# Performance work log

Measured on AMD Instinct MI355X. Metric: run time of the kernel, lower is better.

## Reference

```python
import jax, jax.numpy as jnp
import numpy as np

N, D, H, F = 50000, 128, 8, 512
HD = D // H
EPS_BN = 1e-5


def _batchnorm(x, gamma, beta):
    # BatchNorm1d in training mode: per-feature batch stats over node dim
    m = x.mean(axis=0)
    v = x.var(axis=0)
    return (x - m) * jax.lax.rsqrt(v + EPS_BN) * gamma + beta


def setup_inputs() -> dict:
    key = jax.random.key(0)
    ks = jax.random.split(key, 12)
    s = 0.05
    return {
        "src": jax.random.normal(ks[0], (N, D), jnp.float32),
        "edge_index": jax.random.randint(ks[1], (2, 800000), 0, N, jnp.int64),
        "q_w": jax.random.normal(ks[2], (D, D), jnp.float32) * s,
        "q_b": jnp.zeros((D,), jnp.float32),
        "k_w": jax.random.normal(ks[3], (D, D), jnp.float32) * s,
        "v_w": jax.random.normal(ks[4], (D, D), jnp.float32) * s,
        "out_w": jax.random.normal(ks[5], (D, D), jnp.float32) * s,
        "out_b": jnp.zeros((D,), jnp.float32),
        "g1": jnp.ones((D,), jnp.float32),
        "b1": jnp.zeros((D,), jnp.float32),
        "lin1_w": jax.random.normal(ks[6], (F, D), jnp.float32) * s,
        "lin1_b": jnp.zeros((F,), jnp.float32),
        "lin2_w": jax.random.normal(ks[7], (D, F), jnp.float32) * s,
        "lin2_b": jnp.zeros((D,), jnp.float32),
        "g2": jnp.ones((D,), jnp.float32),
        "b2": jnp.zeros((D,), jnp.float32),
    }


def reference(src, edge_index, q_w, q_b, k_w, v_w, out_w, out_b,
              g1, b1, lin1_w, lin1_b, lin2_w, lin2_b, g2, b2):
    n = src.shape[0]
    # add self loops, then attention edge index is (dst=edge[1], src=edge[0])
    loops = jnp.arange(n, dtype=edge_index.dtype)
    ei = jnp.concatenate([edge_index, jnp.stack([loops, loops])], axis=1)
    e_src, e_dst = ei[0], ei[1]  # message flows e_src -> e_dst; query index = e_dst

    scaling = float(HD) ** (-0.5)
    q = ((src @ q_w.T + q_b) * scaling).reshape(n, H, HD)
    k = (src @ k_w.T).reshape(n, H, HD)
    v = (src @ v_w.T).reshape(n, H, HD)

    # per-edge scores [E, H]
    w = jnp.einsum("ehd,ehd->eh", q[e_dst], k[e_src])
    # deterministic segment softmax over edges grouped by destination node
    mx = jax.ops.segment_max(w, e_dst, num_segments=n)
    ex = jnp.exp(w - mx[e_dst])
    den = jax.ops.segment_sum(ex, e_dst, num_segments=n)
    attn_w = ex / (den[e_dst] + 1e-16)  # [E, H]

    # weighted scatter-add aggregation -> [n, H, HD]
    msgs = attn_w[:, :, None] * v[e_src]
    agg = jax.ops.segment_sum(msgs, e_dst, num_segments=n)

    attn_out = agg.reshape(n, D) @ out_w.T + out_b
    x = _batchnorm(src + attn_out, g1, b1)

    ff = jax.nn.leaky_relu(x @ lin1_w.T + lin1_b, negative_slope=0.01)
    ff = ff @ lin2_w.T + lin2_b
    x = _batchnorm(x + ff, g2, b2)
    return x
```

## Files before the change

kernel.cpp:

```cpp
#include <hip/hip_runtime.h>
#include <math.h>

#define D 128
#define H 8
#define HD 16

typedef __attribute__((ext_vector_type(8))) short bf16x8;
typedef __attribute__((ext_vector_type(4))) float f32x4;

__device__ __forceinline__ ushort f2bf(float x) {
    union { float f; unsigned u; } v; v.f = x;
    unsigned r = v.u + 0x7fffu + ((v.u >> 16) & 1u);
    return (ushort)(r >> 16);
}
__device__ __forceinline__ float bflo(unsigned u) {
    union { unsigned u; float f; } x; x.u = u << 16; return x.f;
}
__device__ __forceinline__ float bfhi(unsigned u) {
    union { unsigned u; float f; } x; x.u = u & 0xffff0000u; return x.f;
}
__device__ __forceinline__ float bf2f(short s) {
    union { unsigned u; float f; } x; x.u = ((unsigned)(ushort)s) << 16; return x.f;
}

__device__ __forceinline__ float dot16(const float* qf, uint4 a, uint4 b) {
    float w;
    w  = qf[0]  * bflo(a.x) + qf[1]  * bfhi(a.x);
    w += qf[2]  * bflo(a.y) + qf[3]  * bfhi(a.y);
    w += qf[4]  * bflo(a.z) + qf[5]  * bfhi(a.z);
    w += qf[6]  * bflo(a.w) + qf[7]  * bfhi(a.w);
    w += qf[8]  * bflo(b.x) + qf[9]  * bfhi(b.x);
    w += qf[10] * bflo(b.y) + qf[11] * bfhi(b.y);
    w += qf[12] * bflo(b.z) + qf[13] * bfhi(b.z);
    w += qf[14] * bflo(b.w) + qf[15] * bfhi(b.w);
    return w;
}
__device__ __forceinline__ void acc16(float* num, float e, uint4 a, uint4 b) {
    num[0]  = fmaf(e, bflo(a.x), num[0]);  num[1]  = fmaf(e, bfhi(a.x), num[1]);
    num[2]  = fmaf(e, bflo(a.y), num[2]);  num[3]  = fmaf(e, bfhi(a.y), num[3]);
    num[4]  = fmaf(e, bflo(a.z), num[4]);  num[5]  = fmaf(e, bfhi(a.z), num[5]);
    num[6]  = fmaf(e, bflo(a.w), num[6]);  num[7]  = fmaf(e, bfhi(a.w), num[7]);
    num[8]  = fmaf(e, bflo(b.x), num[8]);  num[9]  = fmaf(e, bfhi(b.x), num[9]);
    num[10] = fmaf(e, bflo(b.y), num[10]); num[11] = fmaf(e, bfhi(b.y), num[11]);
    num[12] = fmaf(e, bflo(b.z), num[12]); num[13] = fmaf(e, bfhi(b.z), num[13]);
    num[14] = fmaf(e, bflo(b.w), num[14]); num[15] = fmaf(e, bfhi(b.w), num[15]);
}

template<int EPI, int M>
__global__ __launch_bounds__(256)
void gemm_v4_kernel(const ushort* __restrict__ A,
                    const ushort* __restrict__ W,
                    const float* __restrict__ bias,
                    const float* __restrict__ extf,
                    ushort* __restrict__ outb, int N)
{
    const int lane = threadIdx.x & 63, wave = threadIdx.x >> 6;
    const int lr = lane & 15, lq = lane >> 4;
    const int colbase = blockIdx.y * 128 + wave * 32;

    bf16x8 bfr[2][4];
    {
        const ushort* wp = W + (size_t)(colbase + lr) * 128 + lq * 8;
        #pragma unroll
        for (int ct = 0; ct < 2; ++ct)
            #pragma unroll
            for (int t = 0; t < 4; ++t)
                bfr[ct][t] = *(const bf16x8*)(wp + (size_t)ct * 16 * 128 + t * 32);
    }
    float biasv[2];
    biasv[0] = bias[colbase + lr];
    biasv[1] = bias[colbase + 16 + lr];

    const int stride = gridDim.x * 32;
    int r0 = blockIdx.x * 32;
    if (r0 >= N) return;

    bf16x8 cur[2][4], nxt[2][4];
    auto loadA = [&](int rb, bf16x8 (&dst)[2][4]) {
        #pragma unroll
        for (int s = 0; s < 2; ++s) {
            int ar = min(rb + s * 16 + lr, N - 1);
            const ushort* ap = A + (size_t)ar * 128 + lq * 8;
            #pragma unroll
            for (int t = 0; t < 4; ++t)
                dst[s][t] = *(const bf16x8*)(ap + t * 32);
        }
    };
    loadA(r0, cur);

    while (true) {
        int rn = r0 + stride;
        if (rn < N) loadA(rn, nxt);

        f32x4 acc[2][2] = {};
        #pragma unroll
        for (int t = 0; t < 4; ++t) {
            acc[0][0] = __builtin_amdgcn_mfma_f32_16x16x32_bf16(cur[0][t], bfr[0][t], acc[0][0], 0, 0, 0);
            acc[1][0] = __builtin_amdgcn_mfma_f32_16x16x32_bf16(cur[1][t], bfr[0][t], acc[1][0], 0, 0, 0);
            acc[0][1] = __builtin_amdgcn_mfma_f32_16x16x32_bf16(cur[0][t], bfr[1][t], acc[0][1], 0, 0, 0);
            acc[1][1] = __builtin_amdgcn_mfma_f32_16x16x32_bf16(cur[1][t], bfr[1][t], acc[1][1], 0, 0, 0);
        }

        #pragma unroll
        for (int ct = 0; ct < 2; ++ct) {
            int gcol = colbase + ct * 16 + lr;
            #pragma unroll
            for (int s = 0; s < 2; ++s) {
                #pragma unroll
                for (int r = 0; r < 4; ++r) {
                    int grow = r0 + s * 16 + lq * 4 + r;
                    if (grow >= N) continue;
                    size_t o = (size_t)grow * M + gcol;
                    float v = acc[s][ct][r] + biasv[ct];
                    if (EPI == 2)      v = v > 0.f ? v : 0.01f * v;
                    else if (EPI == 3) v += extf[o];
                    outb[o] = f2bf(v);
                }
            }
        }

        if (rn >= N) break;
        r0 = rn;
        #pragma unroll
        for (int s = 0; s < 2; ++s)
            #pragma unroll
            for (int t = 0; t < 4; ++t) cur[s][t] = nxt[s][t];
    }
}

template<int K, int MW>
__global__ __launch_bounds__(256)
void gemm_v2_kernel(const ushort* __restrict__ Ap,
                    const ushort* __restrict__ W,
                    const float* __restrict__ bias,
                    const ushort* __restrict__ extb,
                    const float* __restrict__ rawstats,
                    const float* __restrict__ gg,
                    const float* __restrict__ bb,
                    ushort* __restrict__ outb,
                    int N)
{
    constexpr int M   = MW * 4;
    constexpr int KC  = 128;
    constexpr int KT  = KC / 32;
    constexpr int NKC = K / KC;

    const int lane = threadIdx.x & 63, wave = threadIdx.x >> 6;
    const int lr = lane & 15, lq = lane >> 4;
    const int row0 = blockIdx.x * 32;
    const int c0w  = wave * MW;

    int ar0 = min(row0 + lr, N - 1);
    int ar1 = min(row0 + 16 + lr, N - 1);

    bf16x8 afr[2][KT];
    auto loadA = [&](int kc) {
        #pragma unroll
        for (int s = 0; s < 2; ++s) {
            int ar = s ? ar1 : ar0;
            const ushort* ap = Ap + (size_t)ar * K + kc * KC + lq * 8;
            #pragma unroll
            for (int t = 0; t < KT; ++t) afr[s][t] = *(const bf16x8*)(ap + t * 32);
        }
    };

    f32x4 acc[2][2] = {};
    #pragma unroll 1
    for (int kc = 0; kc < NKC; ++kc) {
        loadA(kc);
        const ushort* wp0 = W + (size_t)(c0w + lr) * K + kc * KC + lq * 8;
        const ushort* wp1 = wp0 + (size_t)16 * K;
        #pragma unroll
        for (int t = 0; t < KT; ++t) {
            bf16x8 b0 = *(const bf16x8*)(wp0 + t * 32);
            bf16x8 b1 = *(const bf16x8*)(wp1 + t * 32);
            acc[0][0] = __builtin_amdgcn_mfma_f32_16x16x32_bf16(afr[0][t], b0, acc[0][0], 0, 0, 0);
            acc[1][0] = __builtin_amdgcn_mfma_f32_16x16x32_bf16(afr[1][t], b0, acc[1][0], 0, 0, 0);
            acc[0][1] = __builtin_amdgcn_mfma_f32_16x16x32_bf16(afr[0][t], b1, acc[0][1], 0, 0, 0);
            acc[1][1] = __builtin_amdgcn_mfma_f32_16x16x32_bf16(afr[1][t], b1, acc[1][1], 0, 0, 0);
        }
    }

    #pragma unroll
    for (int ct = 0; ct < 2; ++ct) {
        int col = c0w + ct * 16 + lr;
        float biasv = bias[col];
        float mean = rawstats[col] / (float)N;
        float var  = rawstats[128 + col] / (float)N - mean * mean;
        float scv = gg[col] * rsqrtf(var + 1e-5f);
        float shv = bb[col] - mean * scv;
        #pragma unroll
        for (int s = 0; s < 2; ++s) {
            #pragma unroll
            for (int r = 0; r < 4; ++r) {
                int grow = row0 + s * 16 + lq * 4 + r;
                if (grow >= N) continue;
                size_t o = (size_t)grow * M + col;
                float v = acc[s][ct][r] + biasv + fmaf(bf2f((short)extb[o]), scv, shv);
                outb[o] = f2bf(v);
            }
        }
    }
}

__global__ __launch_bounds__(256)
void convert_deg_kernel(const float* __restrict__ qw, const float* __restrict__ qb,
                        const float* __restrict__ kw, const float* __restrict__ vw,
                        const float* __restrict__ ow, const float* __restrict__ w1,
                        const float* __restrict__ w2,
                        ushort* __restrict__ wqkv, ushort* __restrict__ wout,
                        ushort* __restrict__ w1b, ushort* __restrict__ w2b,
                        float* __restrict__ bqkv,
                        const float* __restrict__ src, ushort* __restrict__ srcbf,
                        int nd8,
                        const int* __restrict__ ei, long long E0,
                        int* __restrict__ deg)
{
    long long i = (long long)blockIdx.x * 256 + threadIdx.x;
    if (i < E0) atomicAdd(&deg[ei[E0 + i]], 1);
    if (i < nd8) {
        const float4* sp = (const float4*)(src + i * 8);
        float4 f0 = sp[0], f1 = sp[1];
        ushort u[8];
        u[0]=f2bf(f0.x); u[1]=f2bf(f0.y); u[2]=f2bf(f0.z); u[3]=f2bf(f0.w);
        u[4]=f2bf(f1.x); u[5]=f2bf(f1.y); u[6]=f2bf(f1.z); u[7]=f2bf(f1.w);
        *(uint4*)(srcbf + i * 8) = *(uint4*)u;
    }
    if (i < 49152) {
        int row = (int)i >> 7;
        float v;
        if (row < 128)      v = 0.25f * qw[i];
        else if (row < 256) v = kw[i - 16384];
        else                v = vw[i - 32768];
        wqkv[i] = f2bf(v);
        return;
    }
    long long j = i - 49152;
    if (j < 16384) { wout[j] = f2bf(ow[j]); return; }
    j -= 16384;
    if (j < 65536) { w1b[j] = f2bf(w1[j]); return; }
    j -= 65536;
    if (j < 65536) { w2b[j] = f2bf(w2[j]); return; }
    j -= 65536;
    if (j < 384) bqkv[j] = (j < 128) ? 0.25f * qb[j] : 0.f;
}

__global__ __launch_bounds__(256)
void w1fold_kernel(const ushort* __restrict__ w1b, const float* __restrict__ lb1,
                   const float* __restrict__ rawstats,
                   const float* __restrict__ g1, const float* __restrict__ b1,
                   ushort* __restrict__ w1f, float* __restrict__ bias1f, int N)
{
    int f = blockIdx.x * 4 + (threadIdx.x >> 6);
    int lane = threadIdx.x & 63;
    int k0 = lane * 2;
    float m0 = rawstats[k0] / (float)N;
    float v0 = rawstats[128 + k0] / (float)N - m0 * m0;
    float sc0 = g1[k0] * rsqrtf(v0 + 1e-5f);
    float sh0 = b1[k0] - m0 * sc0;
    float m1 = rawstats[k0 + 1] / (float)N;
    float v1 = rawstats[128 + k0 + 1] / (float)N - m1 * m1;
    float sc1 = g1[k0 + 1] * rsqrtf(v1 + 1e-5f);
    float sh1 = b1[k0 + 1] - m1 * sc1;

    uint wp = *(const uint*)(w1b + (size_t)f * 128 + k0);
    float w0 = bflo(wp), w1v = bfhi(wp);
    uint o = (uint)f2bf(w0 * sc0) | ((uint)f2bf(w1v * sc1) << 16);
    *(uint*)(w1f + (size_t)f * 128 + k0) = o;

    float part = w0 * sh0 + w1v * sh1;
    #pragma unroll
    for (int m = 1; m < 64; m <<= 1) part += __shfl_xor(part, m, 64);
    if (lane == 0) bias1f[f] = lb1[f] + part;
}

__global__ __launch_bounds__(256)
void scan_block_sum(const int* __restrict__ deg, int n, int* __restrict__ bsum)
{
    __shared__ int sh[256];
    int i = blockIdx.x * 256 + threadIdx.x;
    sh[threadIdx.x] = (i < n) ? deg[i] : 0;
    __syncthreads();
    for (int ofs = 128; ofs > 0; ofs >>= 1) {
        if (threadIdx.x < ofs) sh[threadIdx.x] += sh[threadIdx.x + ofs];
        __syncthreads();
    }
    if (threadIdx.x == 0) bsum[blockIdx.x] = sh[0];
}

__global__ __launch_bounds__(256)
void scan_final(const int* __restrict__ deg, int n, const int* __restrict__ bsum,
                int nb, int* __restrict__ rowptr)
{
    __shared__ int sb[256];
    __shared__ int sh[256];
    int t = threadIdx.x;
    sb[t] = (t < nb) ? bsum[t] : 0;
    __syncthreads();
    for (int ofs = 1; ofs < 256; ofs <<= 1) {
        int v = (t >= ofs) ? sb[t - ofs] : 0;
        __syncthreads();
        sb[t] += v;
        __syncthreads();
    }
    int boff = (blockIdx.x == 0) ? 0 : sb[blockIdx.x - 1];

    int i = blockIdx.x * 256 + t;
    int v = (i < n) ? deg[i] : 0;
    sh[t] = v;
    __syncthreads();
    for (int ofs = 1; ofs < 256; ofs <<= 1) {
        int u = (t >= ofs) ? sh[t - ofs] : 0;
        __syncthreads();
        sh[t] += u;
        __syncthreads();
    }
    if (i < n) rowptr[i] = boff + sh[t] - v;
    if (i == n - 1) rowptr[n] = boff + sh[t];
}

__global__ __launch_bounds__(256)
void scatter_kernel(const int* __restrict__ ei, long long E0,
                    const int* __restrict__ rowptr, int* __restrict__ cnt,
                    int* __restrict__ col)
{
    long long e = (long long)blockIdx.x * 256 + threadIdx.x;
    if (e >= E0) return;
    int s = ei[e], d = ei[E0 + e];
    int pos = rowptr[d] + atomicAdd(&cnt[d], 1);
    col[pos] = s;
}

__global__ __launch_bounds__(256)
void gat_agg_kernel(const int* __restrict__ rowptr, const int* __restrict__ col,
                    const ushort* __restrict__ qkv, ushort* __restrict__ agg, int N)
{
    int node = blockIdx.x * 4 + (threadIdx.x >> 6);
    if (node >= N) return;
    int lane = threadIdx.x & 63;
    int es = lane >> 3, h = lane & 7;
    const uint4* Q = (const uint4*)qkv;

    const uint4* qp = Q + (size_t)node * 48 + h * 2;
    uint4 qa = qp[0], qb = qp[1];
    float qf[16];
    qf[0]=bflo(qa.x); qf[1]=bfhi(qa.x); qf[2]=bflo(qa.y); qf[3]=bfhi(qa.y);
    qf[4]=bflo(qa.z); qf[5]=bfhi(qa.z); qf[6]=bflo(qa.w); qf[7]=bfhi(qa.w);
    qf[8]=bflo(qb.x); qf[9]=bfhi(qb.x); qf[10]=bflo(qb.y); qf[11]=bfhi(qb.y);
    qf[12]=bflo(qb.z); qf[13]=bfhi(qb.z); qf[14]=bflo(qb.w); qf[15]=bfhi(qb.w);

    float num[16];
    #pragma unroll
    for (int i = 0; i < 16; i++) num[i] = 0.f;
    float den = 0.f;

    int beg = rowptr[node];
    int total = rowptr[node + 1] - beg + 1;
    for (int idx = es; idx < total; idx += 8) {
        int s = (idx == 0) ? node : col[beg + idx - 1];
        const uint4* rp = Q + (size_t)s * 48 + h * 2;
        uint4 ka = rp[16], kb = rp[17], va = rp[32], vb = rp[33];
        float ev = __expf(dot16(qf, ka, kb));
        den += ev;
        acc16(num, ev, va, vb);
    }

    #pragma unroll
    for (int m = 8; m < 64; m <<= 1) {
        den += __shfl_xor(den, m, 64);
        #pragma unroll
        for (int i = 0; i < 16; i++) num[i] += __shfl_xor(num[i], m, 64);
    }

    if (es == 0) {
        float inv = 1.f / (den + 1e-16f);
        uint4 o0, o1;
        o0.x = (uint)f2bf(num[0]*inv)  | ((uint)f2bf(num[1]*inv)  << 16);
        o0.y = (uint)f2bf(num[2]*inv)  | ((uint)f2bf(num[3]*inv)  << 16);
        o0.z = (uint)f2bf(num[4]*inv)  | ((uint)f2bf(num[5]*inv)  << 16);
        o0.w = (uint)f2bf(num[6]*inv)  | ((uint)f2bf(num[7]*inv)  << 16);
        o1.x = (uint)f2bf(num[8]*inv)  | ((uint)f2bf(num[9]*inv)  << 16);
        o1.y = (uint)f2bf(num[10]*inv) | ((uint)f2bf(num[11]*inv) << 16);
        o1.z = (uint)f2bf(num[12]*inv) | ((uint)f2bf(num[13]*inv) << 16);
        o1.w = (uint)f2bf(num[14]*inv) | ((uint)f2bf(num[15]*inv) << 16);
        uint4* op = (uint4*)(agg + (size_t)node * 128 + h * 16);
        op[0] = o0; op[1] = o1;
    }
}

__global__ __launch_bounds__(256)
void bn_stats_bf16_kernel(const ushort* __restrict__ y, int N, float* __restrict__ stats)
{
    int jp = threadIdx.x & 63;
    int q4 = threadIdx.x >> 6;
    int r = blockIdx.x * 256 + q4;
    int rend = min(N, (int)(blockIdx.x + 1) * 256);
    float s0 = 0.f, qq0 = 0.f, s1 = 0.f, qq1 = 0.f;
    const uint* yp = (const uint*)y;
    for (; r < rend; r += 4) {
        uint u = yp[(size_t)r * 64 + jp];
        float a = bflo(u), b = bfhi(u);
        s0 += a; qq0 += a * a; s1 += b; qq1 += b * b;
    }
    __shared__ float sh[4][64][4];
    sh[q4][jp][0] = s0; sh[q4][jp][1] = qq0; sh[q4][jp][2] = s1; sh[q4][jp][3] = qq1;
    __syncthreads();
    if (threadIdx.x < 128) {
        int p = threadIdx.x >> 1;
        int w = threadIdx.x & 1;
        float ss = 0.f, sq = 0.f;
        #pragma unroll
        for (int i = 0; i < 4; i++) { ss += sh[i][p][w * 2]; sq += sh[i][p][w * 2 + 1]; }
        unsafeAtomicAdd(&stats[2 * p + w], ss);
        unsafeAtomicAdd(&stats[128 + 2 * p + w], sq);
    }
}

__global__ __launch_bounds__(256)
void bn_apply_out_kernel(const ushort* __restrict__ y, const float* __restrict__ rawstats,
                         const float* __restrict__ g, const float* __restrict__ b,
                         float* __restrict__ out, int total4, int N)
{
    __shared__ float scs[128], shs[128];
    if (threadIdx.x < 128) {
        int j = threadIdx.x;
        float mean = rawstats[j] / (float)N;
        float var  = rawstats[128 + j] / (float)N - mean * mean;
        float sc = g[j] * rsqrtf(var + 1e-5f);
        scs[j] = sc;
        shs[j] = b[j] - mean * sc;
    }
    __syncthreads();
    int i = blockIdx.x * 256 + threadIdx.x;
    if (i >= total4) return;
    uint2 u = reinterpret_cast<const uint2*>(y)[i];
    int j = (i * 4) & (D - 1);
    float4 v;
    v.x = bflo(u.x) * scs[j + 0] + shs[j + 0];
    v.y = bfhi(u.x) * scs[j + 1] + shs[j + 1];
    v.z = bflo(u.y) * scs[j + 2] + shs[j + 2];
    v.w = bfhi(u.y) * scs[j + 3] + shs[j + 3];
    reinterpret_cast<float4*>(out)[i] = v;
}

extern "C" void kernel_launch(void* const* d_in, const int* in_sizes, int n_in,
                              void* d_out, int out_size, void* d_ws, size_t ws_size,
                              hipStream_t stream)
{
    const float* src    = (const float*)d_in[0];
    const int*   ei     = (const int*)  d_in[1];
    const float* q_w    = (const float*)d_in[2];
    const float* q_b    = (const float*)d_in[3];
    const float* k_w    = (const float*)d_in[4];
    const float* v_w    = (const float*)d_in[5];
    const float* out_w  = (const float*)d_in[6];
    const float* out_b  = (const float*)d_in[7];
    const float* g1     = (const float*)d_in[8];
    const float* b1     = (const float*)d_in[9];
    const float* lin1_w = (const float*)d_in[10];
    const float* lin1_b = (const float*)d_in[11];
    const float* lin2_w = (const float*)d_in[12];
    const float* lin2_b = (const float*)d_in[13];
    const float* g2     = (const float*)d_in[14];
    const float* b2     = (const float*)d_in[15];

    const int N        = in_sizes[0] / D;
    const long long E0 = in_sizes[1] / 2;

    float* ws = (float*)d_ws;
    size_t off = 0;
    ushort* qkv   = (ushort*)(ws + off); off += (size_t)N * 192;
    ushort* agg   = (ushort*)(ws + off); off += (size_t)N * 64;
    ushort* srcbf = (ushort*)(ws + off); off += (size_t)N * 64;
    ushort* y1b   = (ushort*)(ws + off); off += (size_t)N * 64;
    ushort* hid   = (ushort*)(ws + off); off += (size_t)N * 256;
    ushort* y2b   = (ushort*)(ws + off); off += (size_t)N * 64;
    ushort* wqkv  = (ushort*)(ws + off); off += 24576;
    ushort* woutb = (ushort*)(ws + off); off += 8192;
    ushort* w1b   = (ushort*)(ws + off); off += 32768;
    ushort* w1f   = (ushort*)(ws + off); off += 32768;
    ushort* w2b   = (ushort*)(ws + off); off += 32768;
    float*  bqkv  = ws + off;            off += 384;
    float*  bias1f= ws + off;            off += 512;
    size_t zero_start = off;
    int* deg    = (int*)(ws + off); off += N;
    int* cnt    = (int*)(ws + off); off += N;
    float* stats1 = ws + off; off += 512;
    float* stats2 = ws + off; off += 512;
    size_t zero_cnt = off - zero_start;
    int* rowptr = (int*)(ws + off); off += N + 1;
    int* bsum   = (int*)(ws + off); off += 256;
    int* col    = (int*)(ws + off); off += E0;

    hipMemsetAsync(ws + zero_start, 0, zero_cnt * sizeof(float), stream);

    dim3 blk(256);

    dim3 gE0((unsigned)((E0 + 255) / 256));
    hipLaunchKernelGGL(convert_deg_kernel, gE0, blk, 0, stream,
                       q_w, q_b, k_w, v_w, out_w, lin1_w, lin2_w,
                       wqkv, woutb, w1b, w2b, bqkv,
                       src, srcbf, N * 16, ei, E0, deg);

    int nb = (N + 255) / 256;
    hipLaunchKernelGGL(scan_block_sum, dim3(nb), blk, 0, stream, deg, N, bsum);
    hipLaunchKernelGGL(scan_final, dim3(nb), blk, 0, stream, deg, N, bsum, nb, rowptr);
    hipLaunchKernelGGL(scatter_kernel, gE0, blk, 0, stream, ei, E0, rowptr, cnt, col);

    const int gx = 1024;

    hipLaunchKernelGGL((gemm_v4_kernel<0, 384>), dim3(gx, 3), blk, 0, stream,
                       srcbf, wqkv, bqkv, nullptr, qkv, N);

    hipLaunchKernelGGL(gat_agg_kernel, dim3((N + 3) / 4), blk, 0, stream,
                       rowptr, col, qkv, agg, N);

    hipLaunchKernelGGL((gemm_v4_kernel<3, 128>), dim3(gx, 1), blk, 0, stream,
                       agg, woutb, out_b, src, y1b, N);

    dim3 gS((N + 255) / 256);
    hipLaunchKernelGGL(bn_stats_bf16_kernel, gS, blk, 0, stream, y1b, N, stats1);

    hipLaunchKernelGGL(w1fold_kernel, dim3(128), blk, 0, stream,
                       w1b, lin1_b, stats1, g1, b1, w1f, bias1f, N);

    hipLaunchKernelGGL((gemm_v4_kernel<2, 512>), dim3(gx, 4), blk, 0, stream,
                       y1b, w1f, bias1f, nullptr, hid, N);

    hipLaunchKernelGGL((gemm_v2_kernel<512, 32>), dim3((N + 31) / 32), blk, 0, stream,
                       hid, w2b, lin2_b, y1b, stats1, g1, b1, y2b, N);

    hipLaunchKernelGGL(bn_stats_bf16_kernel, gS, blk, 0, stream, y2b, N, stats2);
    int total4 = N * D / 4;
    hipLaunchKernelGGL(bn_apply_out_kernel, dim3((total4 + 255) / 256), blk, 0, stream,
                       y2b, stats2, g2, b2, (float*)d_out, total4, N);
}
```

Measured before the change: 452.5 us.

## Fuse BatchNorm statistics into GEMM epilogues and rewrite lin2 as persistent kernel

Per-column sum and sum-of-squares are now accumulated in the epilogues of the out-projection GEMM and a new lin2 kernel, then reduced with wave shuffles and atomics. This removes both separate bn_stats passes over the bf16 activations. The lin2 GEMM becomes a persistent, grid-strided kernel that keeps all 512 K-values of W in registers and double-buffers A loads, where the old version reloaded weights for every row tile. The stats are taken from the fp32 values before bf16 rounding, so they can differ slightly from statistics computed on the stored bf16 data. Heavier register use may lower occupancy.

```diff
diff --git a/kernel.cpp b/kernel.cpp
--- a/kernel.cpp
+++ b/kernel.cpp
@@ -46,13 +46,15 @@
     num[14] = fmaf(e, bflo(b.w), num[14]); num[15] = fmaf(e, bfhi(b.w), num[15]);
 }
 
-template<int EPI, int M>
+template<int EPI, int M, int STATS>
 __global__ __launch_bounds__(256)
 void gemm_v4_kernel(const ushort* __restrict__ A,
                     const ushort* __restrict__ W,
                     const float* __restrict__ bias,
                     const float* __restrict__ extf,
-                    ushort* __restrict__ outb, int N)
+                    ushort* __restrict__ outb,
+                    float* __restrict__ stats,
+                    int N)
 {
     const int lane = threadIdx.x & 63, wave = threadIdx.x >> 6;
     const int lr = lane & 15, lq = lane >> 4;
@@ -71,135 +73,171 @@
     biasv[0] = bias[colbase + lr];
     biasv[1] = bias[colbase + 16 + lr];
 
+    float ssum[2] = {0.f, 0.f}, ssq[2] = {0.f, 0.f};
+
     const int stride = gridDim.x * 32;
     int r0 = blockIdx.x * 32;
-    if (r0 >= N) return;
-
-    bf16x8 cur[2][4], nxt[2][4];
-    auto loadA = [&](int rb, bf16x8 (&dst)[2][4]) {
-        #pragma unroll
-        for (int s = 0; s < 2; ++s) {
-            int ar = min(rb + s * 16 + lr, N - 1);
-            const ushort* ap = A + (size_t)ar * 128 + lq * 8;
-            #pragma unroll
-            for (int t = 0; t < 4; ++t)
-                dst[s][t] = *(const bf16x8*)(ap + t * 32);
+    if (r0 < N) {
+        bf16x8 cur[2][4], nxt[2][4];
+        auto loadA = [&](int rb, bf16x8 (&dst)[2][4]) {
+            #pragma unroll
+            for (int s = 0; s < 2; ++s) {
+                int ar = min(rb + s * 16 + lr, N - 1);
+                const ushort* ap = A + (size_t)ar * 128 + lq * 8;
+                #pragma unroll
+                for (int t = 0; t < 4; ++t)
+                    dst[s][t] = *(const bf16x8*)(ap + t * 32);
+            }
+        };
+        loadA(r0, cur);
+
+        while (true) {
+            int rn = r0 + stride;
+            if (rn < N) loadA(rn, nxt);
+
+            f32x4 acc[2][2] = {};
+            #pragma unroll
+            for (int t = 0; t < 4; ++t) {
+                acc[0][0] = __builtin_amdgcn_mfma_f32_16x16x32_bf16(cur[0][t], bfr[0][t], acc[0][0], 0, 0, 0);
+                acc[1][0] = __builtin_amdgcn_mfma_f32_16x16x32_bf16(cur[1][t], bfr[0][t], acc[1][0], 0, 0, 0);
+                acc[0][1] = __builtin_amdgcn_mfma_f32_16x16x32_bf16(cur[0][t], bfr[1][t], acc[0][1], 0, 0, 0);
+                acc[1][1] = __builtin_amdgcn_mfma_f32_16x16x32_bf16(cur[1][t], bfr[1][t], acc[1][1], 0, 0, 0);
+            }
+
+            #pragma unroll
+            for (int ct = 0; ct < 2; ++ct) {
+                int gcol = colbase + ct * 16 + lr;
+                #pragma unroll
+                for (int s = 0; s < 2; ++s) {
+                    #pragma unroll
+                    for (int r = 0; r < 4; ++r) {
+                        int grow = r0 + s * 16 + lq * 4 + r;
+                        if (grow >= N) continue;
+                        size_t o = (size_t)grow * M + gcol;
+                        float v = acc[s][ct][r] + biasv[ct];
+                        if (EPI == 2)      v = v > 0.f ? v : 0.01f * v;
+                        else if (EPI == 3) v += extf[o];
+                        if (STATS) { ssum[ct] += v; ssq[ct] = fmaf(v, v, ssq[ct]); }
+                        outb[o] = f2bf(v);
+                    }
+                }
+            }
+
+            if (rn >= N) break;
+            r0 = rn;
+            #pragma unroll
+            for (int s = 0; s < 2; ++s)
+                #pragma unroll
+                for (int t = 0; t < 4; ++t) cur[s][t] = nxt[s][t];
         }
-    };
-    loadA(r0, cur);
-
-    while (true) {
-        int rn = r0 + stride;
-        if (rn < N) loadA(rn, nxt);
-
-        f32x4 acc[2][2] = {};
-        #pragma unroll
-        for (int t = 0; t < 4; ++t) {
-            acc[0][0] = __builtin_amdgcn_mfma_f32_16x16x32_bf16(cur[0][t], bfr[0][t], acc[0][0], 0, 0, 0);
-            acc[1][0] = __builtin_amdgcn_mfma_f32_16x16x32_bf16(cur[1][t], bfr[0][t], acc[1][0], 0, 0, 0);
-            acc[0][1] = __builtin_amdgcn_mfma_f32_16x16x32_bf16(cur[0][t], bfr[1][t], acc[0][1], 0, 0, 0);
-            acc[1][1] = __builtin_amdgcn_mfma_f32_16x16x32_bf16(cur[1][t], bfr[1][t], acc[1][1], 0, 0, 0);
-        }
-
+    }
+
+    if (STATS) {
         #pragma unroll
         for (int ct = 0; ct < 2; ++ct) {
-            int gcol = colbase + ct * 16 + lr;
+            float a = ssum[ct], b = ssq[ct];
+            a += __shfl_xor(a, 16, 64);  b += __shfl_xor(b, 16, 64);
+            a += __shfl_xor(a, 32, 64);  b += __shfl_xor(b, 32, 64);
+            if (lq == 0) {
+                unsafeAtomicAdd(&stats[colbase + ct * 16 + lr], a);
+                unsafeAtomicAdd(&stats[128 + colbase + ct * 16 + lr], b);
+            }
+        }
+    }
+}
+
+#define LIN2_MFMA4(buf, kcb) \
+    acc[0] = __builtin_amdgcn_mfma_f32_16x16x32_bf16(buf[0][0], bfr[(kcb)*4+0], acc[0], 0, 0, 0); \
+    acc[1] = __builtin_amdgcn_mfma_f32_16x16x32_bf16(buf[1][0], bfr[(kcb)*4+0], acc[1], 0, 0, 0); \
+    acc[0] = __builtin_amdgcn_mfma_f32_16x16x32_bf16(buf[0][1], bfr[(kcb)*4+1], acc[0], 0, 0, 0); \
+    acc[1] = __builtin_amdgcn_mfma_f32_16x16x32_bf16(buf[1][1], bfr[(kcb)*4+1], acc[1], 0, 0, 0); \
+    acc[0] = __builtin_amdgcn_mfma_f32_16x16x32_bf16(buf[0][2], bfr[(kcb)*4+2], acc[0], 0, 0, 0); \
+    acc[1] = __builtin_amdgcn_mfma_f32_16x16x32_bf16(buf[1][2], bfr[(kcb)*4+2], acc[1], 0, 0, 0); \
+    acc[0] = __builtin_amdgcn_mfma_f32_16x16x32_bf16(buf[0][3], bfr[(kcb)*4+3], acc[0], 0, 0, 0); \
+    acc[1] = __builtin_amdgcn_mfma_f32_16x16x32_bf16(buf[1][3], bfr[(kcb)*4+3], acc[1], 0, 0, 0);
+
+template<int GX>
+__global__ __launch_bounds__(256, 3)
+void lin2_kernel(const ushort* __restrict__ Ap,
+                 const ushort* __restrict__ W,
+                 const float* __restrict__ bias,
+                 const ushort* __restrict__ extb,
+                 const float* __restrict__ rawstats,
+                 const float* __restrict__ gg,
+                 const float* __restrict__ bb,
+                 ushort* __restrict__ outb,
+                 float* __restrict__ stats2,
+                 int N)
+{
+    const int lane = threadIdx.x & 63, wave = threadIdx.x >> 6;
+    const int lr = lane & 15, lq = lane >> 4;
+    const int col = blockIdx.y * 64 + wave * 16 + lr;
+
+    bf16x8 bfr[16];
+    {
+        const ushort* wp = W + (size_t)col * 512 + lq * 8;
+        #pragma unroll
+        for (int t = 0; t < 16; ++t) bfr[t] = *(const bf16x8*)(wp + t * 32);
+    }
+    float biasv = bias[col];
+    float mean = rawstats[col] / (float)N;
+    float var  = rawstats[128 + col] / (float)N - mean * mean;
+    float scv  = gg[col] * rsqrtf(var + 1e-5f);
+    float shv  = bb[col] - mean * scv;
+
+    float ssum = 0.f, ssq = 0.f;
+
+    const int stride = GX * 32;
+    int r0 = blockIdx.x * 32;
+    if (r0 < N) {
+        bf16x8 bufA[2][4], bufB[2][4];
+        auto loadA = [&](int rb, int kc, bf16x8 (&dst)[2][4]) {
+            #pragma unroll
+            for (int s = 0; s < 2; ++s) {
+                int ar = min(rb + s * 16 + lr, N - 1);
+                const ushort* ap = Ap + (size_t)ar * 512 + kc * 128 + lq * 8;
+                #pragma unroll
+                for (int t = 0; t < 4; ++t)
+                    dst[s][t] = *(const bf16x8*)(ap + t * 32);
+            }
+        };
+        loadA(r0, 0, bufA);
+        while (true) {
+            int rn = r0 + stride;
+            f32x4 acc[2] = {};
+            loadA(r0, 1, bufB);
+            LIN2_MFMA4(bufA, 0)
+            loadA(r0, 2, bufA);
+            LIN2_MFMA4(bufB, 1)
+            loadA(r0, 3, bufB);
+            LIN2_MFMA4(bufA, 2)
+            if (rn < N) loadA(rn, 0, bufA);
+            LIN2_MFMA4(bufB, 3)
+
             #pragma unroll
             for (int s = 0; s < 2; ++s) {
                 #pragma unroll
                 for (int r = 0; r < 4; ++r) {
                     int grow = r0 + s * 16 + lq * 4 + r;
                     if (grow >= N) continue;
-                    size_t o = (size_t)grow * M + gcol;
-                    float v = acc[s][ct][r] + biasv[ct];
-                    if (EPI == 2)      v = v > 0.f ? v : 0.01f * v;
-                    else if (EPI == 3) v += extf[o];
+                    size_t o = (size_t)grow * 128 + col;
+                    float v = acc[s][r] + biasv + fmaf(bf2f((short)extb[o]), scv, shv);
+                    ssum += v;
+                    ssq = fmaf(v, v, ssq);
                     outb[o] = f2bf(v);
                 }
             }
+            if (rn >= N) break;
+            r0 = rn;
         }
-
-        if (rn >= N) break;
-        r0 = rn;
-        #pragma unroll
-        for (int s = 0; s < 2; ++s)
-            #pragma unroll
-            for (int t = 0; t < 4; ++t) cur[s][t] = nxt[s][t];
-    }
-}
-
-template<int K, int MW>
-__global__ __launch_bounds__(256)
-void gemm_v2_kernel(const ushort* __restrict__ Ap,
-                    const ushort* __restrict__ W,
-                    const float* __restrict__ bias,
-                    const ushort* __restrict__ extb,
-                    const float* __restrict__ rawstats,
-                    const float* __restrict__ gg,
-                    const float* __restrict__ bb,
-                    ushort* __restrict__ outb,
-                    int N)
-{
-    constexpr int M   = MW * 4;
-    constexpr int KC  = 128;
-    constexpr int KT  = KC / 32;
-    constexpr int NKC = K / KC;
-
-    const int lane = threadIdx.x & 63, wave = threadIdx.x >> 6;
-    const int lr = lane & 15, lq = lane >> 4;
-    const int row0 = blockIdx.x * 32;
-    const int c0w  = wave * MW;
-
-    int ar0 = min(row0 + lr, N - 1);
-    int ar1 = min(row0 + 16 + lr, N - 1);
-
-    bf16x8 afr[2][KT];
-    auto loadA = [&](int kc) {
-        #pragma unroll
-        for (int s = 0; s < 2; ++s) {
-            int ar = s ? ar1 : ar0;
-            const ushort* ap = Ap + (size_t)ar * K + kc * KC + lq * 8;
-            #pragma unroll
-            for (int t = 0; t < KT; ++t) afr[s][t] = *(const bf16x8*)(ap + t * 32);
-        }
-    };
-
-    f32x4 acc[2][2] = {};
-    #pragma unroll 1
-    for (int kc = 0; kc < NKC; ++kc) {
-        loadA(kc);
-        const ushort* wp0 = W + (size_t)(c0w + lr) * K + kc * KC + lq * 8;
-        const ushort* wp1 = wp0 + (size_t)16 * K;
-        #pragma unroll
-        for (int t = 0; t < KT; ++t) {
-            bf16x8 b0 = *(const bf16x8*)(wp0 + t * 32);
-            bf16x8 b1 = *(const bf16x8*)(wp1 + t * 32);
-            acc[0][0] = __builtin_amdgcn_mfma_f32_16x16x32_bf16(afr[0][t], b0, acc[0][0], 0, 0, 0);
-            acc[1][0] = __builtin_amdgcn_mfma_f32_16x16x32_bf16(afr[1][t], b0, acc[1][0], 0, 0, 0);
-            acc[0][1] = __builtin_amdgcn_mfma_f32_16x16x32_bf16(afr[0][t], b1, acc[0][1], 0, 0, 0);
-            acc[1][1] = __builtin_amdgcn_mfma_f32_16x16x32_bf16(afr[1][t], b1, acc[1][1], 0, 0, 0);
-        }
-    }
-
-    #pragma unroll
-    for (int ct = 0; ct < 2; ++ct) {
-        int col = c0w + ct * 16 + lr;
-        float biasv = bias[col];
-        float mean = rawstats[col] / (float)N;
-        float var  = rawstats[128 + col] / (float)N - mean * mean;
-        float scv = gg[col] * rsqrtf(var + 1e-5f);
-        float shv = bb[col] - mean * scv;
-        #pragma unroll
-        for (int s = 0; s < 2; ++s) {
-            #pragma unroll
-            for (int r = 0; r < 4; ++r) {
-                int grow = row0 + s * 16 + lq * 4 + r;
-                if (grow >= N) continue;
-                size_t o = (size_t)grow * M + col;
-                float v = acc[s][ct][r] + biasv + fmaf(bf2f((short)extb[o]), scv, shv);
-                outb[o] = f2bf(v);
-            }
-        }
+    }
+    ssum += __shfl_xor(ssum, 16, 64);
+    ssq  += __shfl_xor(ssq, 16, 64);
+    ssum += __shfl_xor(ssum, 32, 64);
+    ssq  += __shfl_xor(ssq, 32, 64);
+    if (lq == 0) {
+        unsafeAtomicAdd(&stats2[col], ssum);
+        unsafeAtomicAdd(&stats2[128 + col], ssq);
     }
 }
 
@@ -385,34 +423,6 @@
         o1.w = (uint)f2bf(num[14]*inv) | ((uint)f2bf(num[15]*inv) << 16);
         uint4* op = (uint4*)(agg + (size_t)node * 128 + h * 16);
         op[0] = o0; op[1] = o1;
-    }
-}
-
-__global__ __launch_bounds__(256)
-void bn_stats_bf16_kernel(const ushort* __restrict__ y, int N, float* __restrict__ stats)
-{
-    int jp = threadIdx.x & 63;
-    int q4 = threadIdx.x >> 6;
-    int r = blockIdx.x * 256 + q4;
-    int rend = min(N, (int)(blockIdx.x + 1) * 256);
-    float s0 = 0.f, qq0 = 0.f, s1 = 0.f, qq1 = 0.f;
-    const uint* yp = (const uint*)y;
-    for (; r < rend; r += 4) {
-        uint u = yp[(size_t)r * 64 + jp];
-        float a = bflo(u), b = bfhi(u);
-        s0 += a; qq0 += a * a; s1 += b; qq1 += b * b;
-    }
-    __shared__ float sh[4][64][4];
-    sh[q4][jp][0] = s0; sh[q4][jp][1] = qq0; sh[q4][jp][2] = s1; sh[q4][jp][3] = qq1;
-    __syncthreads();
-    if (threadIdx.x < 128) {
-        int p = threadIdx.x >> 1;
-        int w = threadIdx.x & 1;
-        float ss = 0.f, sq = 0.f;
-        #pragma unroll
-        for (int i = 0; i < 4; i++) { ss += sh[i][p][w * 2]; sq += sh[i][p][w * 2 + 1]; }
-        unsafeAtomicAdd(&stats[2 * p + w], ss);
-        unsafeAtomicAdd(&stats[128 + 2 * p + w], sq);
     }
 }
 
@@ -509,28 +519,24 @@
 
     const int gx = 1024;
 
-    hipLaunchKernelGGL((gemm_v4_kernel<0, 384>), dim3(gx, 3), blk, 0, stream,
-                       srcbf, wqkv, bqkv, nullptr, qkv, N);
+    hipLaunchKernelGGL((gemm_v4_kernel<0, 384, 0>), dim3(gx, 3), blk, 0, stream,
+                       srcbf, wqkv, bqkv, nullptr, qkv, nullptr, N);
 
     hipLaunchKernelGGL(gat_agg_kernel, dim3((N + 3) / 4), blk, 0, stream,
                        rowptr, col, qkv, agg, N);
 
-    hipLaunchKernelGGL((gemm_v4_kernel<3, 128>), dim3(gx, 1), blk, 0, stream,
-                       agg, woutb, out_b, src, y1b, N);
-
-    dim3 gS((N + 255) / 256);
-    hipLaunchKernelGGL(bn_stats_bf16_kernel, gS, blk, 0, stream, y1b, N, stats1);
+    hipLaunchKernelGGL((gemm_v4_kernel<3, 128, 1>), dim3(gx, 1), blk, 0, stream,
+                       agg, woutb, out_b, src, y1b, stats1, N);
 
     hipLaunchKernelGGL(w1fold_kernel, dim3(128), blk, 0, stream,
                        w1b, lin1_b, stats1, g1, b1, w1f, bias1f, N);
 
-    hipLaunchKernelGGL((gemm_v4_kernel<2, 512>), dim3(gx, 4), blk, 0, stream,
-                       y1b, w1f, bias1f, nullptr, hid, N);
-
-    hipLaunchKernelGGL((gemm_v2_kernel<512, 32>), dim3((N + 31) / 32), blk, 0, stream,
-                       hid, w2b, lin2_b, y1b, stats1, g1, b1, y2b, N);
-
-    hipLaunchKernelGGL(bn_stats_bf16_kernel, gS, blk, 0, stream, y2b, N, stats2);
+    hipLaunchKernelGGL((gemm_v4_kernel<2, 512, 0>), dim3(gx, 4), blk, 0, stream,
+                       y1b, w1f, bias1f, nullptr, hid, nullptr, N);
+
+    hipLaunchKernelGGL((lin2_kernel<512>), dim3(512, 2), blk, 0, stream,
+                       hid, w2b, lin2_b, y1b, stats1, g1, b1, y2b, stats2, N);
+
     int total4 = N * D / 4;
     hipLaunchKernelGGL(bn_apply_out_kernel, dim3((total4 + 255) / 256), blk, 0, stream,
                        y2b, stats2, g2, b2, (float*)d_out, total4, N);
```

New measurement: 448.6 us. About the same (-0.8%).

## Fuse BN1 statistics into out-proj GEMM epilogue; halve lin2 GEMM row tile

Applied to the files above, without the earlier changes.

The out-projection GEMM now accumulates per-column sum and sum-of-squares of its fp32 outputs in registers. It reduces them across the wave with shuffles and atomically adds them into stats1, which removes the separate bn_stats pass over y1b. Separately, the lin2 GEMM processes 16 rows per block instead of 32, doubling the grid to raise parallelism at the cost of rereading the weights more often. The stats are now taken from fp32 values rather than the rounded bf16 outputs, and they depend on stats1 being zeroed by the earlier memset.

```diff
diff --git a/kernel.cpp b/kernel.cpp
--- a/kernel.cpp
+++ b/kernel.cpp
@@ -46,13 +46,15 @@
     num[14] = fmaf(e, bflo(b.w), num[14]); num[15] = fmaf(e, bfhi(b.w), num[15]);
 }
 
-template<int EPI, int M>
+template<int EPI, int M, int STATS>
 __global__ __launch_bounds__(256)
 void gemm_v4_kernel(const ushort* __restrict__ A,
                     const ushort* __restrict__ W,
                     const float* __restrict__ bias,
                     const float* __restrict__ extf,
-                    ushort* __restrict__ outb, int N)
+                    ushort* __restrict__ outb,
+                    float* __restrict__ stats,
+                    int N)
 {
     const int lane = threadIdx.x & 63, wave = threadIdx.x >> 6;
     const int lr = lane & 15, lq = lane >> 4;
@@ -71,60 +73,76 @@
     biasv[0] = bias[colbase + lr];
     biasv[1] = bias[colbase + 16 + lr];
 
+    float ssum[2] = {0.f, 0.f}, ssq[2] = {0.f, 0.f};
+
     const int stride = gridDim.x * 32;
     int r0 = blockIdx.x * 32;
-    if (r0 >= N) return;
-
-    bf16x8 cur[2][4], nxt[2][4];
-    auto loadA = [&](int rb, bf16x8 (&dst)[2][4]) {
-        #pragma unroll
-        for (int s = 0; s < 2; ++s) {
-            int ar = min(rb + s * 16 + lr, N - 1);
-            const ushort* ap = A + (size_t)ar * 128 + lq * 8;
-            #pragma unroll
-            for (int t = 0; t < 4; ++t)
-                dst[s][t] = *(const bf16x8*)(ap + t * 32);
-        }
-    };
-    loadA(r0, cur);
-
-    while (true) {
-        int rn = r0 + stride;
-        if (rn < N) loadA(rn, nxt);
-
-        f32x4 acc[2][2] = {};
-        #pragma unroll
-        for (int t = 0; t < 4; ++t) {
-            acc[0][0] = __builtin_amdgcn_mfma_f32_16x16x32_bf16(cur[0][t], bfr[0][t], acc[0][0], 0, 0, 0);
-            acc[1][0] = __builtin_amdgcn_mfma_f32_16x16x32_bf16(cur[1][t], bfr[0][t], acc[1][0], 0, 0, 0);
-            acc[0][1] = __builtin_amdgcn_mfma_f32_16x16x32_bf16(cur[0][t], bfr[1][t], acc[0][1], 0, 0, 0);
-            acc[1][1] = __builtin_amdgcn_mfma_f32_16x16x32_bf16(cur[1][t], bfr[1][t], acc[1][1], 0, 0, 0);
-        }
-
-        #pragma unroll
-        for (int ct = 0; ct < 2; ++ct) {
-            int gcol = colbase + ct * 16 + lr;
+    if (r0 < N) {
+        bf16x8 cur[2][4], nxt[2][4];
+        auto loadA = [&](int rb, bf16x8 (&dst)[2][4]) {
             #pragma unroll
             for (int s = 0; s < 2; ++s) {
+                int ar = min(rb + s * 16 + lr, N - 1);
+                const ushort* ap = A + (size_t)ar * 128 + lq * 8;
                 #pragma unroll
-                for (int r = 0; r < 4; ++r) {
-                    int grow = r0 + s * 16 + lq * 4 + r;
-                    if (grow >= N) continue;
-                    size_t o = (size_t)grow * M + gcol;
-                    float v = acc[s][ct][r] + biasv[ct];
-                    if (EPI == 2)      v = v > 0.f ? v : 0.01f * v;
-                    else if (EPI == 3) v += extf[o];
-                    outb[o] = f2bf(v);
+                for (int t = 0; t < 4; ++t)
+                    dst[s][t] = *(const bf16x8*)(ap + t * 32);
+            }
+        };
+        loadA(r0, cur);
+
+        while (true) {
+            int rn = r0 + stride;
+            if (rn < N) loadA(rn, nxt);
+
+            f32x4 acc[2][2] = {};
+            #pragma unroll
+            for (int t = 0; t < 4; ++t) {
+                acc[0][0] = __builtin_amdgcn_mfma_f32_16x16x32_bf16(cur[0][t], bfr[0][t], acc[0][0], 0, 0, 0);
+                acc[1][0] = __builtin_amdgcn_mfma_f32_16x16x32_bf16(cur[1][t], bfr[0][t], acc[1][0], 0, 0, 0);
+                acc[0][1] = __builtin_amdgcn_mfma_f32_16x16x32_bf16(cur[0][t], bfr[1][t], acc[0][1], 0, 0, 0);
+                acc[1][1] = __builtin_amdgcn_mfma_f32_16x16x32_bf16(cur[1][t], bfr[1][t], acc[1][1], 0, 0, 0);
+            }
+
+            #pragma unroll
+            for (int ct = 0; ct < 2; ++ct) {
+                int gcol = colbase + ct * 16 + lr;
+                #pragma unroll
+                for (int s = 0; s < 2; ++s) {
+                    #pragma unroll
+                    for (int r = 0; r < 4; ++r) {
+                        int grow = r0 + s * 16 + lq * 4 + r;
+                        if (grow >= N) continue;
+                        size_t o = (size_t)grow * M + gcol;
+                        float v = acc[s][ct][r] + biasv[ct];
+                        if (EPI == 2)      v = v > 0.f ? v : 0.01f * v;
+                        else if (EPI == 3) v += extf[o];
+                        if (STATS) { ssum[ct] += v; ssq[ct] = fmaf(v, v, ssq[ct]); }
+                        outb[o] = f2bf(v);
+                    }
                 }
             }
+
+            if (rn >= N) break;
+            r0 = rn;
+            #pragma unroll
+            for (int s = 0; s < 2; ++s)
+                #pragma unroll
+                for (int t = 0; t < 4; ++t) cur[s][t] = nxt[s][t];
         }
-
-        if (rn >= N) break;
-        r0 = rn;
-        #pragma unroll
-        for (int s = 0; s < 2; ++s)
-            #pragma unroll
-            for (int t = 0; t < 4; ++t) cur[s][t] = nxt[s][t];
+    }
+
+    if (STATS) {
+        #pragma unroll
+        for (int ct = 0; ct < 2; ++ct) {
+            float a = ssum[ct], b = ssq[ct];
+            a += __shfl_xor(a, 16, 64);  b += __shfl_xor(b, 16, 64);
+            a += __shfl_xor(a, 32, 64);  b += __shfl_xor(b, 32, 64);
+            if (lq == 0) {
+                unsafeAtomicAdd(&stats[colbase + ct * 16 + lr], a);
+                unsafeAtomicAdd(&stats[128 + colbase + ct * 16 + lr], b);
+            }
+        }
     }
 }
 
@@ -147,24 +165,19 @@
 
     const int lane = threadIdx.x & 63, wave = threadIdx.x >> 6;
     const int lr = lane & 15, lq = lane >> 4;
-    const int row0 = blockIdx.x * 32;
+    const int row0 = blockIdx.x * 16;
     const int c0w  = wave * MW;
 
     int ar0 = min(row0 + lr, N - 1);
-    int ar1 = min(row0 + 16 + lr, N - 1);
-
-    bf16x8 afr[2][KT];
+
+    bf16x8 afr[KT];
     auto loadA = [&](int kc) {
-        #pragma unroll
-        for (int s = 0; s < 2; ++s) {
-            int ar = s ? ar1 : ar0;
-            const ushort* ap = Ap + (size_t)ar * K + kc * KC + lq * 8;
-            #pragma unroll
-            for (int t = 0; t < KT; ++t) afr[s][t] = *(const bf16x8*)(ap + t * 32);
-        }
+        const ushort* ap = Ap + (size_t)ar0 * K + kc * KC + lq * 8;
+        #pragma unroll
+        for (int t = 0; t < KT; ++t) afr[t] = *(const bf16x8*)(ap + t * 32);
     };
 
-    f32x4 acc[2][2] = {};
+    f32x4 acc[2] = {};
     #pragma unroll 1
     for (int kc = 0; kc < NKC; ++kc) {
         loadA(kc);
@@ -174,10 +187,8 @@
         for (int t = 0; t < KT; ++t) {
             bf16x8 b0 = *(const bf16x8*)(wp0 + t * 32);
             bf16x8 b1 = *(const bf16x8*)(wp1 + t * 32);
-            acc[0][0] = __builtin_amdgcn_mfma_f32_16x16x32_bf16(afr[0][t], b0, acc[0][0], 0, 0, 0);
-            acc[1][0] = __builtin_amdgcn_mfma_f32_16x16x32_bf16(afr[1][t], b0, acc[1][0], 0, 0, 0);
-            acc[0][1] = __builtin_amdgcn_mfma_f32_16x16x32_bf16(afr[0][t], b1, acc[0][1], 0, 0, 0);
-            acc[1][1] = __builtin_amdgcn_mfma_f32_16x16x32_bf16(afr[1][t], b1, acc[1][1], 0, 0, 0);
+            acc[0] = __builtin_amdgcn_mfma_f32_16x16x32_bf16(afr[t], b0, acc[0], 0, 0, 0);
+            acc[1] = __builtin_amdgcn_mfma_f32_16x16x32_bf16(afr[t], b1, acc[1], 0, 0, 0);
         }
     }
 
@@ -190,15 +201,12 @@
         float scv = gg[col] * rsqrtf(var + 1e-5f);
         float shv = bb[col] - mean * scv;
         #pragma unroll
-        for (int s = 0; s < 2; ++s) {
-            #pragma unroll
-            for (int r = 0; r < 4; ++r) {
-                int grow = row0 + s * 16 + lq * 4 + r;
-                if (grow >= N) continue;
-                size_t o = (size_t)grow * M + col;
-                float v = acc[s][ct][r] + biasv + fmaf(bf2f((short)extb[o]), scv, shv);
-                outb[o] = f2bf(v);
-            }
+        for (int r = 0; r < 4; ++r) {
+            int grow = row0 + lq * 4 + r;
+            if (grow >= N) continue;
+            size_t o = (size_t)grow * M + col;
+            float v = acc[ct][r] + biasv + fmaf(bf2f((short)extb[o]), scv, shv);
+            outb[o] = f2bf(v);
         }
     }
 }
@@ -509,27 +517,25 @@
 
     const int gx = 1024;
 
-    hipLaunchKernelGGL((gemm_v4_kernel<0, 384>), dim3(gx, 3), blk, 0, stream,
-                       srcbf, wqkv, bqkv, nullptr, qkv, N);
+    hipLaunchKernelGGL((gemm_v4_kernel<0, 384, 0>), dim3(gx, 3), blk, 0, stream,
+                       srcbf, wqkv, bqkv, nullptr, qkv, nullptr, N);
 
     hipLaunchKernelGGL(gat_agg_kernel, dim3((N + 3) / 4), blk, 0, stream,
                        rowptr, col, qkv, agg, N);
 
-    hipLaunchKernelGGL((gemm_v4_kernel<3, 128>), dim3(gx, 1), blk, 0, stream,
-                       agg, woutb, out_b, src, y1b, N);
-
-    dim3 gS((N + 255) / 256);
-    hipLaunchKernelGGL(bn_stats_bf16_kernel, gS, blk, 0, stream, y1b, N, stats1);
+    hipLaunchKernelGGL((gemm_v4_kernel<3, 128, 1>), dim3(gx, 1), blk, 0, stream,
+                       agg, woutb, out_b, src, y1b, stats1, N);
 
     hipLaunchKernelGGL(w1fold_kernel, dim3(128), blk, 0, stream,
                        w1b, lin1_b, stats1, g1, b1, w1f, bias1f, N);
 
-    hipLaunchKernelGGL((gemm_v4_kernel<2, 512>), dim3(gx, 4), blk, 0, stream,
-                       y1b, w1f, bias1f, nullptr, hid, N);
-
-    hipLaunchKernelGGL((gemm_v2_kernel<512, 32>), dim3((N + 31) / 32), blk, 0, stream,
+    hipLaunchKernelGGL((gemm_v4_kernel<2, 512, 0>), dim3(gx, 4), blk, 0, stream,
+                       y1b, w1f, bias1f, nullptr, hid, nullptr, N);
+
+    hipLaunchKernelGGL((gemm_v2_kernel<512, 32>), dim3((N + 15) / 16), blk, 0, stream,
                        hid, w2b, lin2_b, y1b, stats1, g1, b1, y2b, N);
 
+    dim3 gS((N + 255) / 256);
     hipLaunchKernelGGL(bn_stats_bf16_kernel, gS, blk, 0, stream, y2b, N, stats2);
     int total4 = N * D / 4;
     hipLaunchKernelGGL(bn_apply_out_kernel, dim3((total4 + 255) / 256), blk, 0, stream,
```

New measurement: 463.5 us. 1.02x slower.
